# Performance work log

Hardware: AMD Instinct MI355X
Metric: run time of the kernel (lower is better)

The kernel has to match this reference:

```python
import jax, jax.numpy as jnp
import numpy as np

N_NODES = 100000
N_GRAPHS = 512
D_IN = 300
D_HID = 300
D_OUT = 128  # 2 * SEQUENCE_LENGTH


def _gcn_norm(edge_index, n):
    # PyG GCNConv default: add self-loops, symmetric normalization
    src, dst = edge_index[0], edge_index[1]
    loop = jnp.arange(n, dtype=src.dtype)
    src = jnp.concatenate([src, loop])
    dst = jnp.concatenate([dst, loop])
    deg = jax.ops.segment_sum(jnp.ones_like(dst, dtype=jnp.float32), dst, num_segments=n)
    dinv = jnp.where(deg > 0, jax.lax.rsqrt(deg), 0.0)
    norm = dinv[src] * dinv[dst]  # [E+N]
    return src, dst, norm


def _gcn_conv(x, src, dst, norm, W, b, n):
    h = x @ W                              # transform first (PyG order)
    msg = norm[:, None] * h[src]           # gather + scale, [E+N, D]
    agg = jax.ops.segment_sum(msg, dst, num_segments=n)  # scatter-add
    return agg + b


def setup_inputs() -> dict:
    key = jax.random.key(0)
    ks = jax.random.split(key, 10)
    x = jax.random.normal(ks[0], (N_NODES, D_IN), dtype=jnp.float32)
    edge_index = jax.random.randint(ks[1], (2, 800000), 0, N_NODES, dtype=jnp.int64)
    batch = jnp.sort(jax.random.randint(ks[2], (N_NODES,), 0, N_GRAPHS, dtype=jnp.int64))
    s = 1.0 / np.sqrt(D_IN)
    W1 = jax.random.uniform(ks[3], (D_IN, D_HID), jnp.float32, -s, s)
    b1 = jnp.zeros((D_HID,), jnp.float32)
    W2 = jax.random.uniform(ks[4], (D_HID, D_HID), jnp.float32, -s, s)
    b2 = jnp.zeros((D_HID,), jnp.float32)
    W3 = jax.random.uniform(ks[5], (D_HID, D_OUT), jnp.float32, -s, s)
    b3 = jnp.zeros((D_OUT,), jnp.float32)
    Wm = jax.random.uniform(ks[6], (D_OUT, 1), jnp.float32, -s, s)
    bm = jnp.zeros((1,), jnp.float32)
    return {"x": x, "edge_index": edge_index, "batch": batch,
            "W1": W1, "b1": b1, "W2": W2, "b2": b2,
            "W3": W3, "b3": b3, "Wm": Wm, "bm": bm}


def reference(x, edge_index, batch, W1, b1, W2, b2, W3, b3, Wm, bm):
    n = x.shape[0]
    src, dst, norm = _gcn_norm(edge_index, n)
    # dropout is identity in eval mode
    h = jax.nn.relu(_gcn_conv(x, src, dst, norm, W1, b1, n))
    h = jax.nn.relu(_gcn_conv(h, src, dst, norm, W2, b2, n))
    h = jax.nn.relu(_gcn_conv(h, src, dst, norm, W3, b3, n))
    # global mean pool over graphs
    sums = jax.ops.segment_sum(h, batch, num_segments=N_GRAPHS)
    cnt = jax.ops.segment_sum(jnp.ones((n,), jnp.float32), batch, num_segments=N_GRAPHS)
    readout = sums / jnp.maximum(cnt, 1.0)[:, None]   # [G, D_OUT]
    return (readout @ Wm + bm)[:, 0]                  # [G]
```

## Files before the change

### kernel.cpp

```cpp
#include <hip/hip_runtime.h>
#include <hip/hip_bf16.h>

typedef __bf16 bf16;
typedef __bf16 bf16x4 __attribute__((ext_vector_type(4)));
typedef __bf16 bf16x8 __attribute__((ext_vector_type(8)));
typedef float f32x4 __attribute__((ext_vector_type(4)));

constexpr int N_NODES  = 100000;
constexpr int N_EDGES  = 800000;
constexpr int N_GRAPHS = 512;
constexpr int D_IN  = 300;
constexpr int D_HID = 300;
constexpr int D_OUT = 128;
constexpr int KP    = 320;
constexpr int MT    = 128;
constexpr int NTILE = (N_NODES + MT - 1) / MT;
constexpr int NPAD  = NTILE * MT;

#define AS1(p) ((const __attribute__((address_space(1))) void*)(p))
#define AS3(p) ((__attribute__((address_space(3))) void*)(p))


__global__ __launch_bounds__(256) void k_init(int* deg, float* gsum, int* cnt) {
  int i = blockIdx.x * 256 + threadIdx.x;
  if (i < N_NODES) deg[i] = 0;
  if (i < N_GRAPHS) { gsum[i] = 0.f; cnt[i] = 0; }
}

__global__ __launch_bounds__(256) void k_deg(const int* __restrict__ ei, int* __restrict__ deg) {
  int e4 = blockIdx.x * 256 + threadIdx.x;
  if (e4 < N_EDGES / 4) {
    int4 d4 = ((const int4*)(ei + N_EDGES))[e4];
    atomicAdd(&deg[d4.x], 1);
    atomicAdd(&deg[d4.y], 1);
    atomicAdd(&deg[d4.z], 1);
    atomicAdd(&deg[d4.w], 1);
  }
}

__global__ __launch_bounds__(256) void k_scan1(const int* __restrict__ deg, int* __restrict__ rp,
                                               int* __restrict__ part) {
  __shared__ int sm[256];
  int tid = threadIdx.x;
  int i = blockIdx.x * 256 + tid;
  int v = (i < N_NODES) ? deg[i] : 0;
  sm[tid] = v;
  __syncthreads();
  for (int off = 1; off < 256; off <<= 1) {
    int t = (tid >= off) ? sm[tid - off] : 0;
    __syncthreads();
    sm[tid] += t;
    __syncthreads();
  }
  if (i < N_NODES) rp[i] = sm[tid] - v;
  if (tid == 255) part[blockIdx.x] = sm[255];
}

__global__ __launch_bounds__(512) void k_scan2(int* part, int nb) {
  __shared__ int sm[512];
  int tid = threadIdx.x;
  int v = (tid < nb) ? part[tid] : 0;
  sm[tid] = v;
  __syncthreads();
  for (int off = 1; off < 512; off <<= 1) {
    int t = (tid >= off) ? sm[tid - off] : 0;
    __syncthreads();
    sm[tid] += t;
    __syncthreads();
  }
  if (tid < nb) part[tid] = sm[tid] - v;
}

__global__ __launch_bounds__(256) void k_scan3(int* __restrict__ rp, const int* __restrict__ part,
                                               int* __restrict__ cur, const int* __restrict__ deg,
                                               float* __restrict__ dinv) {
  int i = blockIdx.x * 256 + threadIdx.x;
  if (i < N_NODES) {
    int r = rp[i] + part[blockIdx.x];
    rp[i] = r;
    cur[i] = r;
    dinv[i] = rsqrtf((float)(deg[i] + 1));
  }
  if (i == 0) rp[N_NODES] = N_EDGES;
}

__global__ __launch_bounds__(256) void k_fill(const int* __restrict__ ei, int* __restrict__ cur,
                                              int* __restrict__ col) {
  int e4 = blockIdx.x * 256 + threadIdx.x;
  if (e4 < N_EDGES / 4) {
    int4 s4 = ((const int4*)ei)[e4];
    int4 d4 = ((const int4*)(ei + N_EDGES))[e4];
    col[atomicAdd(&cur[d4.x], 1)] = s4.x;
    col[atomicAdd(&cur[d4.y], 1)] = s4.y;
    col[atomicAdd(&cur[d4.z], 1)] = s4.z;
    col[atomicAdd(&cur[d4.w], 1)] = s4.w;
  }
}


__global__ __launch_bounds__(256) void k_conv_x(const float* __restrict__ x, const float* __restrict__ dinv,
                                                bf16* __restrict__ Xs) {
  int i = blockIdx.x * 256 + threadIdx.x;
  if (i >= N_NODES * (KP / 4)) return;
  int j = i % (KP / 4);
  int v = i / (KP / 4);
  float4 f = make_float4(0.f, 0.f, 0.f, 0.f);
  if (j < D_IN / 4) f = ((const float4*)(x + (size_t)v * D_IN))[j];
  float dv = dinv[v];
  bf16x4 o;
  o[0] = (bf16)(f.x * dv); o[1] = (bf16)(f.y * dv); o[2] = (bf16)(f.z * dv); o[3] = (bf16)(f.w * dv);
  *(bf16x4*)(Xs + (size_t)v * KP + j * 4) = o;
}

__global__ __launch_bounds__(256) void k_conv_w_all(const float* __restrict__ W1, const float* __restrict__ W2,
                                                    const float* __restrict__ W3, bf16* __restrict__ Wt) {
  int i = blockIdx.x * 256 + threadIdx.x;
  if (i >= 3 * KP * KP) return;
  int w = i / (KP * KP);
  int r = i % (KP * KP);
  int k = r % KP;
  int n = r / KP;
  float f = 0.f;
  if (w == 0)      { if (k < 300 && n < 300) f = W1[k * 300 + n]; }
  else if (w == 1) { if (k < 300 && n < 300) f = W2[k * 300 + n]; }
  else             { if (k < 300 && n < 128) f = W3[k * 128 + n]; }
  Wt[i] = (bf16)f;
}


__global__ __launch_bounds__(256) void k_aggb(const bf16* __restrict__ in, const int* __restrict__ rp,
                                              const int* __restrict__ col, const float* __restrict__ dinv,
                                              bf16* __restrict__ out) {
  int w = threadIdx.x >> 6, l = threadIdx.x & 63;
  int v = blockIdx.x * 4 + w;
  if (v >= N_NODES) return;
  if (l >= 40) return;
  const size_t co = (size_t)8 * l;

  float A0[8], A1[8];
  {
    bf16x8 p = *(const bf16x8*)(in + (size_t)v * KP + co);
#pragma unroll
    for (int j = 0; j < 8; ++j) { A0[j] = (float)p[j]; A1[j] = 0.f; }
  }
  int s = rp[v], e = rp[v + 1];
  int i = s;
  for (; i + 4 <= e; i += 4) {
    int u0 = col[i], u1 = col[i + 1], u2 = col[i + 2], u3 = col[i + 3];
    bf16x8 p0 = *(const bf16x8*)(in + (size_t)u0 * KP + co);
    bf16x8 p1 = *(const bf16x8*)(in + (size_t)u1 * KP + co);
    bf16x8 p2 = *(const bf16x8*)(in + (size_t)u2 * KP + co);
    bf16x8 p3 = *(const bf16x8*)(in + (size_t)u3 * KP + co);
#pragma unroll
    for (int j = 0; j < 8; ++j) {
      A0[j] += (float)p0[j] + (float)p2[j];
      A1[j] += (float)p1[j] + (float)p3[j];
    }
  }
  for (; i + 2 <= e; i += 2) {
    int u0 = col[i], u1 = col[i + 1];
    bf16x8 p0 = *(const bf16x8*)(in + (size_t)u0 * KP + co);
    bf16x8 p1 = *(const bf16x8*)(in + (size_t)u1 * KP + co);
#pragma unroll
    for (int j = 0; j < 8; ++j) { A0[j] += (float)p0[j]; A1[j] += (float)p1[j]; }
  }
  if (i < e) {
    int u0 = col[i];
    bf16x8 p0 = *(const bf16x8*)(in + (size_t)u0 * KP + co);
#pragma unroll
    for (int j = 0; j < 8; ++j) A0[j] += (float)p0[j];
  }
  float dv = dinv[v];
  bf16x8 o;
#pragma unroll
  for (int j = 0; j < 8; ++j) o[j] = (bf16)((A0[j] + A1[j]) * dv);
  *(bf16x8*)(out + (size_t)v * KP + co) = o;
}


__global__ __launch_bounds__(256) void k_agg3(const bf16* __restrict__ T3, const int* __restrict__ rp,
                                              const int* __restrict__ col, const float* __restrict__ dinv,
                                              const float* __restrict__ bias, const float* __restrict__ Wm,
                                              float* __restrict__ sArr) {
  const int tid = threadIdx.x;
  const int c = tid & 15;
  const int v = blockIdx.x * 16 + (tid >> 4);
  const size_t co = (size_t)8 * c;

  float A0[8], A1[8];
  {
    bf16x8 p = *(const bf16x8*)(T3 + (size_t)v * 128 + co);
#pragma unroll
    for (int j = 0; j < 8; ++j) { A0[j] = (float)p[j]; A1[j] = 0.f; }
  }
  int s = rp[v], e = rp[v + 1];
  int i = s;
  for (; i + 4 <= e; i += 4) {
    int u0 = col[i], u1 = col[i + 1], u2 = col[i + 2], u3 = col[i + 3];
    bf16x8 p0 = *(const bf16x8*)(T3 + (size_t)u0 * 128 + co);
    bf16x8 p1 = *(const bf16x8*)(T3 + (size_t)u1 * 128 + co);
    bf16x8 p2 = *(const bf16x8*)(T3 + (size_t)u2 * 128 + co);
    bf16x8 p3 = *(const bf16x8*)(T3 + (size_t)u3 * 128 + co);
#pragma unroll
    for (int j = 0; j < 8; ++j) {
      A0[j] += (float)p0[j] + (float)p2[j];
      A1[j] += (float)p1[j] + (float)p3[j];
    }
  }
  for (; i + 2 <= e; i += 2) {
    int u0 = col[i], u1 = col[i + 1];
    bf16x8 p0 = *(const bf16x8*)(T3 + (size_t)u0 * 128 + co);
    bf16x8 p1 = *(const bf16x8*)(T3 + (size_t)u1 * 128 + co);
#pragma unroll
    for (int j = 0; j < 8; ++j) { A0[j] += (float)p0[j]; A1[j] += (float)p1[j]; }
  }
  if (i < e) {
    bf16x8 p0 = *(const bf16x8*)(T3 + (size_t)col[i] * 128 + co);
#pragma unroll
    for (int j = 0; j < 8; ++j) A0[j] += (float)p0[j];
  }

  float dv = dinv[v];
  float sv = 0.f;
#pragma unroll
  for (int j = 0; j < 8; ++j) {
    int d = (int)co + j;
    float val = fmaxf((A0[j] + A1[j]) * dv + bias[d], 0.f);
    sv += val * Wm[d];
  }
#pragma unroll
  for (int m = 1; m < 16; m <<= 1) sv += __shfl_xor(sv, m);
  if (c == 0) sArr[v] = sv;
}


template <int NP, int WM, int WN, int EPI>
__global__ __launch_bounds__(512, 4) void k_gemm(const bf16* __restrict__ A, const bf16* __restrict__ Bt,
                                                 const float* __restrict__ dinv, const float* __restrict__ bias,
                                                 bf16* __restrict__ H) {
  constexpr int WROWS = MT / WM;
  constexpr int MI    = WROWS / 16;
  constexpr int WCOLS = NP / WN;
  constexpr int NC    = WCOLS / 16;
  constexpr int NB_B  = NP / 64;
  __shared__ __attribute__((aligned(16))) char sA[MT * 128];
  __shared__ __attribute__((aligned(16))) char sB[NP * 128];

  const int tid = threadIdx.x;
  const int w = tid >> 6, l = tid & 63;
  const int wm = w / WN, wn = w % WN;
  const int m0 = blockIdx.x * MT;

  const int sr  = tid >> 3;
  const int ssw = ((tid & 7) << 4) ^ ((sr & 7) << 4);
  const char* Ab = (const char*)A;
  const char* Bb = (const char*)Bt;

  const int la = l & 15, q = l >> 4;
  const int msk = (la & 7) << 4;

  f32x4 acc[MI][NC] = {};

  for (int kh = 0; kh < 5; ++kh) {
#pragma unroll
    for (int i = 0; i < 2; ++i) {
      const char* src = Ab + (size_t)(m0 + i * 64 + sr) * 640 + kh * 128 + ssw;
      __builtin_amdgcn_global_load_lds(AS1(src), AS3(sA + i * 8192 + w * 1024), 16, 0, 0);
    }
#pragma unroll
    for (int i = 0; i < NB_B; ++i) {
      const char* src = Bb + (size_t)(i * 64 + sr) * 640 + kh * 128 + ssw;
      __builtin_amdgcn_global_load_lds(AS1(src), AS3(sB + i * 8192 + w * 1024), 16, 0, 0);
    }
    __syncthreads();

#pragma unroll
    for (int ks = 0; ks < 2; ++ks) {
      const int cb = (ks * 64 + q * 16) ^ msk;
      bf16x8 af[MI];
#pragma unroll
      for (int mi = 0; mi < MI; ++mi) {
        int r = wm * WROWS + mi * 16 + la;
        af[mi] = *(const bf16x8*)(sA + r * 128 + cb);
      }
#pragma unroll
      for (int nc = 0; nc < NC; ++nc) {
        int rb = wn * WCOLS + nc * 16 + la;
        bf16x8 bfr = *(const bf16x8*)(sB + rb * 128 + cb);
#pragma unroll
        for (int mi = 0; mi < MI; ++mi)
          acc[mi][nc] = __builtin_amdgcn_mfma_f32_16x16x32_bf16(af[mi], bfr, acc[mi][nc], 0, 0, 0);
      }
    }
    __syncthreads();
  }

  const int rbase = m0 + wm * WROWS + q * 4;
  if (EPI == 0) {
    float bc[NC];
#pragma unroll
    for (int nc = 0; nc < NC; ++nc) {
      int c = wn * WCOLS + nc * 16 + la;
      bc[nc] = (c < D_HID) ? bias[c] : 0.f;
    }
#pragma unroll
    for (int mi = 0; mi < MI; ++mi) {
#pragma unroll
      for (int r = 0; r < 4; ++r) {
        int row = rbase + mi * 16 + r;
        if (row < N_NODES) {
          float dv = dinv[row];
#pragma unroll
          for (int nc = 0; nc < NC; ++nc) {
            int c = wn * WCOLS + nc * 16 + la;
            H[(size_t)row * KP + c] = (bf16)(fmaxf(acc[mi][nc][r] + bc[nc], 0.f) * dv);
          }
        }
      }
    }
  } else {
#pragma unroll
    for (int mi = 0; mi < MI; ++mi) {
#pragma unroll
      for (int r = 0; r < 4; ++r) {
        int row = rbase + mi * 16 + r;
        if (row < N_NODES) {
#pragma unroll
          for (int nc = 0; nc < NC; ++nc) {
            int c = wn * WCOLS + nc * 16 + la;
            H[(size_t)row * NP + c] = (bf16)acc[mi][nc][r];
          }
        }
      }
    }
  }
}


__global__ __launch_bounds__(256) void k_gsum(const float* __restrict__ sArr, const int* __restrict__ batch,
                                              float* __restrict__ gsum, int* __restrict__ cnt) {
  __shared__ float lsum[N_GRAPHS];
  __shared__ int   lcnt[N_GRAPHS];
  int tid = threadIdx.x;
  lsum[tid] = 0.f; lsum[tid + 256] = 0.f;
  lcnt[tid] = 0;   lcnt[tid + 256] = 0;
  __syncthreads();
  int v = blockIdx.x * 256 + tid;
  if (v < N_NODES) {
    int b = batch[v];
    atomicAdd(&lsum[b], sArr[v]);
    atomicAdd(&lcnt[b], 1);
  }
  __syncthreads();
  int v0 = blockIdx.x * 256;
  int v1 = min(v0 + 255, N_NODES - 1);
  int g0 = batch[v0], g1 = batch[v1];
  for (int g = g0 + tid; g <= g1; g += 256) {
    int c = lcnt[g];
    if (c) { atomicAdd(&gsum[g], lsum[g]); atomicAdd(&cnt[g], c); }
  }
}

__global__ __launch_bounds__(512) void k_final(const float* __restrict__ gsum, const int* __restrict__ cnt,
                                               const float* __restrict__ bm, float* __restrict__ out) {
  int g = blockIdx.x * 512 + threadIdx.x;
  if (g < N_GRAPHS) out[g] = gsum[g] / fmaxf((float)cnt[g], 1.f) + bm[0];
}


extern "C" void kernel_launch(void* const* d_in, const int* in_sizes, int n_in,
                              void* d_out, int out_size, void* d_ws, size_t ws_size,
                              hipStream_t stream) {
  const float* x    = (const float*)d_in[0];
  const int*   ei   = (const int*)d_in[1];
  const int*   batch= (const int*)d_in[2];
  const float* W1   = (const float*)d_in[3];
  const float* b1   = (const float*)d_in[4];
  const float* W2   = (const float*)d_in[5];
  const float* b2   = (const float*)d_in[6];
  const float* W3   = (const float*)d_in[7];
  const float* b3   = (const float*)d_in[8];
  const float* Wm   = (const float*)d_in[9];
  const float* bm   = (const float*)d_in[10];
  float* out = (float*)d_out;

  char* ws = (char*)d_ws;
  size_t off = 0;
  auto alloc = [&](size_t bytes) {
    void* p = ws + off;
    off = (off + bytes + 255) & ~(size_t)255;
    return p;
  };
  bf16*  Xs   = (bf16*)alloc((size_t)NPAD * KP * sizeof(bf16));
  bf16*  Ab   = (bf16*)alloc((size_t)NPAD * KP * sizeof(bf16));
  bf16*  T3   = (bf16*)alloc((size_t)NPAD * 128 * sizeof(bf16));
  bf16*  Wt   = (bf16*)alloc((size_t)3 * KP * KP * sizeof(bf16));
  int*   deg  = (int*)alloc((size_t)N_NODES * 4);
  float* dinv = (float*)alloc((size_t)N_NODES * 4);
  int*   rp   = (int*)alloc((size_t)(N_NODES + 1) * 4);
  int*   cur  = (int*)alloc((size_t)N_NODES * 4);
  int*   col  = (int*)alloc((size_t)N_EDGES * 4);
  int*   part = (int*)alloc(1024 * 4);
  float* sArr = (float*)alloc((size_t)N_NODES * 4);
  float* gsum = (float*)alloc((size_t)N_GRAPHS * 4);
  int*   cnt  = (int*)alloc((size_t)N_GRAPHS * 4);
  bf16*  H    = Xs;
  bf16*  Wt1  = Wt;
  bf16*  Wt2  = Wt + (size_t)KP * KP;
  bf16*  Wt3  = Wt + (size_t)2 * KP * KP;

  int nbN = (N_NODES + 255) / 256;
  int nbE4 = (N_EDGES / 4 + 255) / 256;
  int nbA = (N_NODES + 3) / 4;
  int nbWall = (3 * KP * KP + 255) / 256;

  k_init<<<nbN, 256, 0, stream>>>(deg, gsum, cnt);
  k_deg<<<nbE4, 256, 0, stream>>>(ei, deg);
  k_conv_w_all<<<nbWall, 256, 0, stream>>>(W1, W2, W3, Wt);
  k_scan1<<<nbN, 256, 0, stream>>>(deg, rp, part);
  k_scan2<<<1, 512, 0, stream>>>(part, nbN);
  k_scan3<<<nbN, 256, 0, stream>>>(rp, part, cur, deg, dinv);
  k_fill<<<nbE4, 256, 0, stream>>>(ei, cur, col);
  k_conv_x<<<(N_NODES * (KP / 4) + 255) / 256, 256, 0, stream>>>(x, dinv, Xs);

  k_aggb<<<nbA, 256, 0, stream>>>(Xs, rp, col, dinv, Ab);
  k_gemm<KP, 2, 4, 0><<<NTILE, 512, 0, stream>>>(Ab, Wt1, dinv, b1, H);
  k_aggb<<<nbA, 256, 0, stream>>>(H, rp, col, dinv, Ab);
  k_gemm<KP, 2, 4, 0><<<NTILE, 512, 0, stream>>>(Ab, Wt2, dinv, b2, H);
  k_gemm<128, 8, 1, 1><<<NTILE, 512, 0, stream>>>(H, Wt3, dinv, nullptr, T3);
  k_agg3<<<N_NODES / 16, 256, 0, stream>>>(T3, rp, col, dinv, b3, Wm, sArr);

  k_gsum<<<nbN, 256, 0, stream>>>(sArr, batch, gsum, cnt);
  k_final<<<1, 512, 0, stream>>>(gsum, cnt, bm, out);
}
```

Baseline: 441.8 us.

## Fuse fp32 input conversion into first GEMM and reorder layer-1 transform before aggregation

Removes the separate pass that converts x to scaled bf16. A new GEMM kernel reads the fp32 features directly, converts them to bf16 into LDS, multiplies by W1 and applies the dinv scale in its epilogue. Layer 1 now transforms before aggregating, and the layer-1 aggregation applies bias, ReLU and the dinv prescale for layer 2 in its epilogue. This drops one full read/write pass over the node features and one launch, at the cost of a GEMM without cross-iteration pipelining and more per-element epilogue work in aggregation.

New measurement: 484.5 us. 9.7% more time.

```diff
diff --git a/kernel.cpp b/kernel.cpp
--- a/kernel.cpp
+++ b/kernel.cpp
@@ -95,21 +95,6 @@
     col[atomicAdd(&cur[d4.z], 1)] = s4.z;
     col[atomicAdd(&cur[d4.w], 1)] = s4.w;
   }
-}
-
-
-__global__ __launch_bounds__(256) void k_conv_x(const float* __restrict__ x, const float* __restrict__ dinv,
-                                                bf16* __restrict__ Xs) {
-  int i = blockIdx.x * 256 + threadIdx.x;
-  if (i >= N_NODES * (KP / 4)) return;
-  int j = i % (KP / 4);
-  int v = i / (KP / 4);
-  float4 f = make_float4(0.f, 0.f, 0.f, 0.f);
-  if (j < D_IN / 4) f = ((const float4*)(x + (size_t)v * D_IN))[j];
-  float dv = dinv[v];
-  bf16x4 o;
-  o[0] = (bf16)(f.x * dv); o[1] = (bf16)(f.y * dv); o[2] = (bf16)(f.z * dv); o[3] = (bf16)(f.w * dv);
-  *(bf16x4*)(Xs + (size_t)v * KP + j * 4) = o;
 }
 
 __global__ __launch_bounds__(256) void k_conv_w_all(const float* __restrict__ W1, const float* __restrict__ W2,
@@ -128,9 +113,99 @@
 }
 
 
+__global__ __launch_bounds__(512, 4) void k_gemm1(const float* __restrict__ X, const bf16* __restrict__ Bt,
+                                                  const float* __restrict__ dinv, bf16* __restrict__ T1) {
+  constexpr int MI = 4, NC = 5, NB_B = 5;
+  __shared__ __attribute__((aligned(16))) char sA[MT * 128];
+  __shared__ __attribute__((aligned(16))) char sB[KP * 128];
+
+  const int tid = threadIdx.x;
+  const int w = tid >> 6, l = tid & 63;
+  const int wm = w / 4, wn = w % 4;
+  const int m0 = blockIdx.x * MT;
+
+  const int sr  = tid >> 3;
+  const int ssw = ((tid & 7) << 4) ^ ((sr & 7) << 4);
+  const char* Bb = (const char*)Bt;
+
+  const int arow = tid >> 2;
+  const int cg   = tid & 3;
+  int rA = m0 + arow;
+  if (rA > N_NODES - 1) rA = N_NODES - 1;
+  const float* xrow = X + (size_t)rA * D_IN;
+  char* aw0 = sA + arow * 128 + ((cg * 32 +  0) ^ ((arow & 7) << 4));
+  char* aw1 = sA + arow * 128 + ((cg * 32 + 16) ^ ((arow & 7) << 4));
+
+  const int la = l & 15, q = l >> 4;
+  const int msk = (la & 7) << 4;
+
+  f32x4 acc[MI][NC] = {};
+
+  for (int kh = 0; kh < 5; ++kh) {
+    float4 f[4];
+#pragma unroll
+    for (int j = 0; j < 4; ++j) {
+      int f4i = kh * 16 + cg * 4 + j;
+      f[j] = (f4i < 75) ? ((const float4*)xrow)[f4i] : make_float4(0.f, 0.f, 0.f, 0.f);
+    }
+    bf16x8 h0, h1;
+    h0[0]=(bf16)f[0].x; h0[1]=(bf16)f[0].y; h0[2]=(bf16)f[0].z; h0[3]=(bf16)f[0].w;
+    h0[4]=(bf16)f[1].x; h0[5]=(bf16)f[1].y; h0[6]=(bf16)f[1].z; h0[7]=(bf16)f[1].w;
+    h1[0]=(bf16)f[2].x; h1[1]=(bf16)f[2].y; h1[2]=(bf16)f[2].z; h1[3]=(bf16)f[2].w;
+    h1[4]=(bf16)f[3].x; h1[5]=(bf16)f[3].y; h1[6]=(bf16)f[3].z; h1[7]=(bf16)f[3].w;
+    *(bf16x8*)aw0 = h0;
+    *(bf16x8*)aw1 = h1;
+#pragma unroll
+    for (int i = 0; i < NB_B; ++i) {
+      const char* src = Bb + (size_t)(i * 64 + sr) * 640 + kh * 128 + ssw;
+      __builtin_amdgcn_global_load_lds(AS1(src), AS3(sB + i * 8192 + w * 1024), 16, 0, 0);
+    }
+    __syncthreads();
+
+#pragma unroll
+    for (int ks = 0; ks < 2; ++ks) {
+      const int cb = (ks * 64 + q * 16) ^ msk;
+      bf16x8 af[MI];
+#pragma unroll
+      for (int mi = 0; mi < MI; ++mi) {
+        int r = wm * 64 + mi * 16 + la;
+        af[mi] = *(const bf16x8*)(sA + r * 128 + cb);
+      }
+#pragma unroll
+      for (int nc = 0; nc < NC; ++nc) {
+        int rb = wn * 80 + nc * 16 + la;
+        bf16x8 bfr = *(const bf16x8*)(sB + rb * 128 + cb);
+#pragma unroll
+        for (int mi = 0; mi < MI; ++mi)
+          acc[mi][nc] = __builtin_amdgcn_mfma_f32_16x16x32_bf16(af[mi], bfr, acc[mi][nc], 0, 0, 0);
+      }
+    }
+    __syncthreads();
+  }
+
+  const int rbase = m0 + wm * 64 + q * 4;
+#pragma unroll
+  for (int mi = 0; mi < MI; ++mi) {
+#pragma unroll
+    for (int r = 0; r < 4; ++r) {
+      int row = rbase + mi * 16 + r;
+      if (row < N_NODES) {
+        float dv = dinv[row];
+#pragma unroll
+        for (int nc = 0; nc < NC; ++nc) {
+          int c = wn * 80 + nc * 16 + la;
+          T1[(size_t)row * KP + c] = (bf16)(acc[mi][nc][r] * dv);
+        }
+      }
+    }
+  }
+}
+
+
+template <int EPI>
 __global__ __launch_bounds__(256) void k_aggb(const bf16* __restrict__ in, const int* __restrict__ rp,
                                               const int* __restrict__ col, const float* __restrict__ dinv,
-                                              bf16* __restrict__ out) {
+                                              const float* __restrict__ bias, bf16* __restrict__ out) {
   int w = threadIdx.x >> 6, l = threadIdx.x & 63;
   int v = blockIdx.x * 4 + w;
   if (v >= N_NODES) return;
@@ -173,7 +248,16 @@
   float dv = dinv[v];
   bf16x8 o;
 #pragma unroll
-  for (int j = 0; j < 8; ++j) o[j] = (bf16)((A0[j] + A1[j]) * dv);
+  for (int j = 0; j < 8; ++j) {
+    float sum = (A0[j] + A1[j]) * dv;
+    if (EPI == 0) {
+      o[j] = (bf16)sum;
+    } else {
+      int d = (int)co + j;
+      float val = (d < D_HID) ? fmaxf(sum + bias[d], 0.f) * dv : 0.f;
+      o[j] = (bf16)val;
+    }
+  }
   *(bf16x8*)(out + (size_t)v * KP + co) = o;
 }
 
@@ -391,8 +475,8 @@
     off = (off + bytes + 255) & ~(size_t)255;
     return p;
   };
-  bf16*  Xs   = (bf16*)alloc((size_t)NPAD * KP * sizeof(bf16));
-  bf16*  Ab   = (bf16*)alloc((size_t)NPAD * KP * sizeof(bf16));
+  bf16*  bufA = (bf16*)alloc((size_t)NPAD * KP * sizeof(bf16));
+  bf16*  bufB = (bf16*)alloc((size_t)NPAD * KP * sizeof(bf16));
   bf16*  T3   = (bf16*)alloc((size_t)NPAD * 128 * sizeof(bf16));
   bf16*  Wt   = (bf16*)alloc((size_t)3 * KP * KP * sizeof(bf16));
   int*   deg  = (int*)alloc((size_t)N_NODES * 4);
@@ -404,7 +488,6 @@
   float* sArr = (float*)alloc((size_t)N_NODES * 4);
   float* gsum = (float*)alloc((size_t)N_GRAPHS * 4);
   int*   cnt  = (int*)alloc((size_t)N_GRAPHS * 4);
-  bf16*  H    = Xs;
   bf16*  Wt1  = Wt;
   bf16*  Wt2  = Wt + (size_t)KP * KP;
   bf16*  Wt3  = Wt + (size_t)2 * KP * KP;
@@ -421,13 +504,12 @@
   k_scan2<<<1, 512, 0, stream>>>(part, nbN);
   k_scan3<<<nbN, 256, 0, stream>>>(rp, part, cur, deg, dinv);
   k_fill<<<nbE4, 256, 0, stream>>>(ei, cur, col);
-  k_conv_x<<<(N_NODES * (KP / 4) + 255) / 256, 256, 0, stream>>>(x, dinv, Xs);
-
-  k_aggb<<<nbA, 256, 0, stream>>>(Xs, rp, col, dinv, Ab);
-  k_gemm<KP, 2, 4, 0><<<NTILE, 512, 0, stream>>>(Ab, Wt1, dinv, b1, H);
-  k_aggb<<<nbA, 256, 0, stream>>>(H, rp, col, dinv, Ab);
-  k_gemm<KP, 2, 4, 0><<<NTILE, 512, 0, stream>>>(Ab, Wt2, dinv, b2, H);
-  k_gemm<128, 8, 1, 1><<<NTILE, 512, 0, stream>>>(H, Wt3, dinv, nullptr, T3);
+
+  k_gemm1<<<NTILE, 512, 0, stream>>>(x, Wt1, dinv, bufA);
+  k_aggb<1><<<nbA, 256, 0, stream>>>(bufA, rp, col, dinv, b1, bufB);
+  k_aggb<0><<<nbA, 256, 0, stream>>>(bufB, rp, col, dinv, nullptr, bufA);
+  k_gemm<KP, 2, 4, 0><<<NTILE, 512, 0, stream>>>(bufA, Wt2, dinv, b2, bufB);
+  k_gemm<128, 8, 1, 1><<<NTILE, 512, 0, stream>>>(bufB, Wt3, dinv, nullptr, T3);
   k_agg3<<<N_NODES / 16, 256, 0, stream>>>(T3, rp, col, dinv, b3, Wm, sArr);
 
   k_gsum<<<nbN, 256, 0, stream>>>(sArr, batch, gsum, cnt);
```
